# Optimization experiments

Measured on AMD Instinct MI355X. Metric: run time of the kernel, lower is better.

## Reference

```python
import jax, jax.numpy as jnp
import numpy as np

D_MODEL = 1024
N_HEADS = 16
SEQ = 2048
BATCH = 2
EPS = 1e-5


def layer_norm(x, g, b):
    mu = jnp.mean(x, axis=-1, keepdims=True)
    var = jnp.mean(jnp.square(x - mu), axis=-1, keepdims=True)
    return (x - mu) * jax.lax.rsqrt(var + EPS) * g + b


def setup_inputs() -> dict:
    key = jax.random.key(0)
    ks = jax.random.split(key, 10)
    D = D_MODEL
    s = lambda fan_in: 1.0 / np.sqrt(fan_in)
    return {
        "x": jax.random.normal(ks[0], (BATCH, SEQ, D), dtype=jnp.float32),
        # weights stored [in, out] (torch Linear is y = x @ W.T; equivalent math)
        "w_attn": jax.random.uniform(ks[1], (D, 3 * D), minval=-s(D), maxval=s(D), dtype=jnp.float32),
        "b_attn": jnp.zeros((3 * D,), jnp.float32),
        "w_proj": jax.random.uniform(ks[2], (D, D), minval=-s(D), maxval=s(D), dtype=jnp.float32),
        "b_proj": jnp.zeros((D,), jnp.float32),
        "ln1_g": jnp.ones((D,), jnp.float32),
        "ln1_b": jnp.zeros((D,), jnp.float32),
        "ln2_g": jnp.ones((D,), jnp.float32),
        "ln2_b": jnp.zeros((D,), jnp.float32),
        "w_fc1": jax.random.uniform(ks[3], (D, 4 * D), minval=-s(D), maxval=s(D), dtype=jnp.float32),
        "b_fc1": jnp.zeros((4 * D,), jnp.float32),
        "w_fc2": jax.random.uniform(ks[4], (4 * D, D), minval=-s(4 * D), maxval=s(4 * D), dtype=jnp.float32),
        "b_fc2": jnp.zeros((D,), jnp.float32),
    }


def reference(x, w_attn, b_attn, w_proj, b_proj, ln1_g, ln1_b, ln2_g, ln2_b, w_fc1, b_fc1, w_fc2, b_fc2):
    B, L, D = x.shape
    H = N_HEADS
    Dh = D // H

    # --- attention sublayer ---
    h = layer_norm(x, ln1_g, ln1_b)
    qkv = h @ w_attn + b_attn                      # [B, L, 3D]
    # SOURCE BUG (faithful): q, k, v are all taken from the k third.
    k = qkv[..., D:2 * D]
    kh = k.reshape(B, L, H, Dh).transpose(0, 2, 1, 3)   # [B, H, L, Dh]
    att = jnp.einsum('bhqd,bhkd->bhqk', kh, kh) / jnp.sqrt(jnp.float32(Dh))
    att = jax.nn.softmax(att, axis=-1)
    out = jnp.einsum('bhqk,bhkd->bhqd', att, kh)         # [B, H, L, Dh]
    out = out.transpose(0, 2, 1, 3).reshape(B, L, D)
    x = x + (out @ w_proj + b_proj)

    # --- feed-forward sublayer ---
    h = layer_norm(x, ln2_g, ln2_b)
    h = jax.nn.relu(h @ w_fc1 + b_fc1)
    x = x + (h @ w_fc2 + b_fc2)
    return x
```

## Files before the change

### kernel.cpp

```cpp
#include <hip/hip_runtime.h>


typedef __attribute__((ext_vector_type(8))) short s8v;
typedef __attribute__((ext_vector_type(4))) short s4v;
typedef __attribute__((ext_vector_type(4))) float f4v;

#define D_MODEL 1024
#define SEQ 2048
#define BATCH 2
#define NH 16
#define DH 64
#define MROWS (BATCH * SEQ)

#define KH_SCALE 0.42466088f
#define KH_ISCALE 2.3548200f

__device__ __forceinline__ float b2f(unsigned short u) {
  union { unsigned int i; float f; } v; v.i = ((unsigned int)u) << 16; return v.f;
}
__device__ __forceinline__ unsigned short f2b(float f) {
  unsigned int i = __builtin_bit_cast(unsigned int, f);
  unsigned int r = (i + 0x7fffu + ((i >> 16) & 1u)) >> 16;
  return (unsigned short)r;
}
__device__ __forceinline__ void async16(const void* g, void* l) {
  __builtin_amdgcn_global_load_lds(
      (const __attribute__((address_space(1))) unsigned int*)g,
      (__attribute__((address_space(3))) unsigned int*)l, 16, 0, 0);
}
__device__ __forceinline__ unsigned short cvt_b(float f) { return f2b(f); }
__device__ __forceinline__ unsigned short cvt_b(unsigned short u) { return u; }

__device__ __forceinline__ float xp2(float x) {
#if __has_builtin(__builtin_amdgcn_exp2f)
  return __builtin_amdgcn_exp2f(x);
#else
  return exp2f(x);
#endif
}

__device__ __forceinline__ s4v cvt4(float a, float b, float c, float d) {
  unsigned int lo, hi;
  asm("v_cvt_pk_bf16_f32 %0, %1, %2" : "=v"(lo) : "v"(a), "v"(b));
  asm("v_cvt_pk_bf16_f32 %0, %1, %2" : "=v"(hi) : "v"(c), "v"(d));
  union { unsigned long long u; s4v v; } u;
  u.u = ((unsigned long long)hi << 32) | (unsigned long long)lo;
  return u.v;
}

#if __has_builtin(__builtin_amdgcn_mfma_f32_16x16x16_bf16)
__device__ __forceinline__ f4v mfma16(s4v a, s4v b, f4v c) {
  return __builtin_amdgcn_mfma_f32_16x16x16_bf16(a, b, c, 0, 0, 0);
}
#elif __has_builtin(__builtin_amdgcn_mfma_f32_16x16x16bf16_1k)
__device__ __forceinline__ f4v mfma16(s4v a, s4v b, f4v c) {
  return __builtin_amdgcn_mfma_f32_16x16x16bf16_1k(a, b, c, 0, 0, 0);
}
#else
__device__ __forceinline__ f4v mfma16(s4v a, s4v b, f4v c) {
  s8v aa = {a[0], a[1], a[2], a[3], 0, 0, 0, 0};
  s8v bb = {b[0], b[1], b[2], b[3], 0, 0, 0, 0};
  return __builtin_amdgcn_mfma_f32_16x16x32_bf16(aa, bb, c, 0, 0, 0);
}
#endif

__global__ __launch_bounds__(256) void ln_kernel(
    const float* __restrict__ x, const float* __restrict__ g,
    const float* __restrict__ bb, unsigned short* __restrict__ out) {
  int row = blockIdx.x;
  int t = threadIdx.x;
  const float* xr = x + (size_t)row * D_MODEL;
  float v[4];
  float s = 0.f, s2 = 0.f;
#pragma unroll
  for (int i = 0; i < 4; ++i) {
    float f = xr[t + 256 * i];
    v[i] = f; s += f; s2 += f * f;
  }
#pragma unroll
  for (int off = 1; off < 64; off <<= 1) {
    s += __shfl_xor(s, off, 64);
    s2 += __shfl_xor(s2, off, 64);
  }
  __shared__ float red[8];
  if ((t & 63) == 0) { red[t >> 6] = s; red[4 + (t >> 6)] = s2; }
  __syncthreads();
  s = red[0] + red[1] + red[2] + red[3];
  s2 = red[4] + red[5] + red[6] + red[7];
  float mu = s * (1.f / D_MODEL);
  float var = s2 * (1.f / D_MODEL) - mu * mu;
  float rstd = rsqrtf(var + 1e-5f);
#pragma unroll
  for (int i = 0; i < 4; ++i) {
    int c = t + 256 * i;
    float h = (v[i] - mu) * rstd * g[c] + bb[c];
    out[(size_t)row * D_MODEL + c] = f2b(h);
  }
}

template <typename T>
__global__ __launch_bounds__(256) void transpose_b(
    const T* __restrict__ src, unsigned short* __restrict__ dst,
    int srcStride, int dstStride, long long srcBatch, long long dstBatch) {
  __shared__ unsigned short tile[64][65];
  const T* s = src + (size_t)blockIdx.z * srcBatch;
  unsigned short* d = dst + (size_t)blockIdx.z * dstBatch;
  int n0 = blockIdx.x * 64, k0 = blockIdx.y * 64;
  for (int i = threadIdx.x; i < 4096; i += 256) {
    int k = i >> 6, n = i & 63;
    tile[k][n] = cvt_b(s[(size_t)(k0 + k) * srcStride + n0 + n]);
  }
  __syncthreads();
  for (int i = threadIdx.x; i < 4096; i += 256) {
    int n = i >> 6, k = i & 63;
    d[(size_t)(n0 + n) * dstStride + k0 + k] = tile[k][n];
  }
}

template <int RES, bool RELU, bool KH, int OUTF, int BM, int BN>
__global__ __launch_bounds__(256) void gemm_bt(
    const unsigned short* __restrict__ A, const unsigned short* __restrict__ Bt,
    const float* __restrict__ bias, const float* __restrict__ res,
    void* __restrict__ out, int M, int N, int K) {
  constexpr int MT = BM / 32;
  constexpr int NT = BN / 32;
  __shared__ __align__(16) unsigned short lsA[2][BM * 64];
  __shared__ __align__(16) unsigned short lsB[2][BN * 64];
  int tid = threadIdx.x;
  int lane = tid & 63, w = tid >> 6, quad = lane >> 4, l16 = lane & 15;
  int m0 = blockIdx.y * BM, n0 = blockIdx.x * BN;
  int wm = (w >> 1) * (BM / 2), wn = (w & 1) * (BN / 2);
  f4v acc[MT][NT] = {};

  auto stage = [&](int bsel, int ktE) {
#pragma unroll
    for (int i = 0; i < MT; ++i) {
      int cb = w * (BM * 2) + i * 64;
      int ci = cb + lane;
      int row = ci >> 3, c = ci & 7;
      int cs = c ^ (row & 7);
      async16(A + (size_t)(m0 + row) * K + ktE + cs * 8, &lsA[bsel][cb * 8]);
    }
#pragma unroll
    for (int i = 0; i < NT; ++i) {
      int cb = w * (BN * 2) + i * 64;
      int ci = cb + lane;
      int row = ci >> 3, c = ci & 7;
      int cs = c ^ (row & 7);
      async16(Bt + (size_t)(n0 + row) * K + ktE + cs * 8, &lsB[bsel][cb * 8]);
    }
  };

  stage(0, 0);
  int nK = K >> 6;
  for (int kt = 0; kt < nK; ++kt) {
    int b = kt & 1;
    if (kt + 1 < nK) {
      stage(b ^ 1, (kt + 1) << 6);
      if constexpr (MT + NT == 4)      asm volatile("s_waitcnt vmcnt(4)" ::: "memory");
      else if constexpr (MT + NT == 6) asm volatile("s_waitcnt vmcnt(6)" ::: "memory");
      else                             asm volatile("s_waitcnt vmcnt(8)" ::: "memory");
    } else {
      asm volatile("s_waitcnt vmcnt(0)" ::: "memory");
    }
    __builtin_amdgcn_sched_barrier(0);
    __builtin_amdgcn_s_barrier();
    __builtin_amdgcn_sched_barrier(0);
#pragma unroll
    for (int s = 0; s < 2; ++s) {
      s8v af[MT], bf[NT];
#pragma unroll
      for (int t = 0; t < MT; ++t) {
        int am = wm + t * 16 + l16;
        int ac = (s * 4 + quad) ^ (am & 7);
        af[t] = *(const s8v*)(&lsA[b][am * 64 + ac * 8]);
      }
#pragma unroll
      for (int t = 0; t < NT; ++t) {
        int bn = wn + t * 16 + l16;
        int bc = (s * 4 + quad) ^ (bn & 7);
        bf[t] = *(const s8v*)(&lsB[b][bn * 64 + bc * 8]);
      }
#pragma unroll
      for (int ti = 0; ti < MT; ++ti)
#pragma unroll
        for (int tj = 0; tj < NT; ++tj)
          acc[ti][tj] = __builtin_amdgcn_mfma_f32_16x16x32_bf16(
              af[ti], bf[tj], acc[ti][tj], 0, 0, 0);
    }
    asm volatile("s_waitcnt lgkmcnt(0)" ::: "memory");
    __builtin_amdgcn_sched_barrier(0);
    __builtin_amdgcn_s_barrier();
    __builtin_amdgcn_sched_barrier(0);
  }
#pragma unroll
  for (int tj = 0; tj < NT; ++tj) {
    int col = n0 + wn + tj * 16 + l16;
    float bv = bias[col];
#pragma unroll
    for (int ti = 0; ti < MT; ++ti) {
#pragma unroll
      for (int r = 0; r < 4; ++r) {
        int rowg = m0 + wm + ti * 16 + quad * 4 + r;
        float vv = acc[ti][tj][r] + bv;
        if (KH) vv *= KH_SCALE;
        if (RES == 2) vv += res[(size_t)rowg * N + col];
        if (RELU) vv = fmaxf(vv, 0.f);
        size_t oidx;
        if (KH) {
          int b2 = rowg >> 11, l = rowg & 2047, h = col >> 6, d = col & 63;
          oidx = (((size_t)(b2 * NH + h)) * SEQ + l) * DH + d;
        } else {
          oidx = (size_t)rowg * N + col;
        }
        if (OUTF == 0) ((unsigned short*)out)[oidx] = f2b(vv);
        else           ((float*)out)[oidx] = vv;
      }
    }
  }
}

__global__ __launch_bounds__(256) void flash_k(
    const unsigned short* __restrict__ kh, const unsigned short* __restrict__ khT,
    unsigned short* __restrict__ Opart, float* __restrict__ lpart) {
  __shared__ __align__(16) unsigned short lsK[128 * 64];
  __shared__ __align__(16) unsigned short lsKT[64 * 128];
  int tid = threadIdx.x;
  int lane = tid & 63, w = tid >> 6, quad = lane >> 4, l16 = lane & 15;
  int split = blockIdx.x, bh = blockIdx.y, qb = blockIdx.z;
  const unsigned short* khB = kh + (size_t)bh * SEQ * DH;
  const unsigned short* khTB = khT + (size_t)bh * DH * SEQ;
  unsigned short* Op = Opart + (size_t)split * MROWS * D_MODEL;
  float* lp = lpart + (size_t)split * BATCH * NH * SEQ;
  s8v aQ[2][2];
#pragma unroll
  for (int g = 0; g < 2; ++g) {
    int q = qb * 128 + w * 32 + g * 16 + l16;
#pragma unroll
    for (int s = 0; s < 2; ++s)
      aQ[g][s] = *(const s8v*)(khB + (size_t)q * DH + s * 32 + quad * 8);
  }
  const s4v vone = {(short)0x3F80, (short)0x3F80, (short)0x3F80, (short)0x3F80};
  f4v accO[2][4] = {};
  f4v accL[2] = {};

  for (int kt8 = 0; kt8 < 8; ++kt8) {
    int key0 = split * 1024 + kt8 * 128;
#pragma unroll
    for (int i = 0; i < 4; ++i) {
      int cb = w * 256 + i * 64;
      int ci = cb + lane;
      int row = ci >> 3, c = ci & 7;
      int cs = c ^ (row & 7);
      async16(khB + (size_t)(key0 + row) * DH + cs * 8, &lsK[cb * 8]);
    }
#pragma unroll
    for (int i = 0; i < 4; ++i) {
      int cb = w * 256 + i * 64;
      int ci = cb + lane;
      int row = ci >> 4, c = ci & 15;
      int cs = c ^ (row & 15);
      async16(khTB + (size_t)row * SEQ + key0 + cs * 8, &lsKT[cb * 8]);
    }
    __builtin_amdgcn_s_waitcnt(0x0f70);
    __syncthreads();
#pragma unroll
    for (int half = 0; half < 2; ++half) {
      f4v accST[2][4] = {};
#pragma unroll
      for (int s = 0; s < 2; ++s) {
#pragma unroll
        for (int tj = 0; tj < 4; ++tj) {
          int key = half * 64 + tj * 16 + l16;
          int c = (s * 4 + quad) ^ (key & 7);
          s8v kf = *(const s8v*)(&lsK[key * 64 + c * 8]);
#pragma unroll
          for (int g = 0; g < 2; ++g)
            accST[g][tj] = __builtin_amdgcn_mfma_f32_16x16x32_bf16(
                kf, aQ[g][s], accST[g][tj], 0, 0, 0);
        }
      }
#pragma unroll
      for (int tj = 0; tj < 4; ++tj) {
        s4v pf[2];
#pragma unroll
        for (int g = 0; g < 2; ++g) {
          float p0 = xp2(accST[g][tj][0]);
          float p1 = xp2(accST[g][tj][1]);
          float p2 = xp2(accST[g][tj][2]);
          float p3 = xp2(accST[g][tj][3]);
          pf[g] = cvt4(p0, p1, p2, p3);
          accL[g] = mfma16(pf[g], vone, accL[g]);
        }
#pragma unroll
        for (int db = 0; db < 4; ++db) {
          int d = db * 16 + l16;
          int ch = (half * 8 + tj * 2 + (quad >> 1)) ^ (d & 15);
          s4v vf = *(const s4v*)(&lsKT[d * 128 + ch * 8 + (quad & 1) * 4]);
#pragma unroll
          for (int g = 0; g < 2; ++g)
            accO[g][db] = mfma16(pf[g], vf, accO[g][db]);
        }
      }
    }
    __syncthreads();
  }
  int b = bh >> 4, h = bh & 15;
#pragma unroll
  for (int g = 0; g < 2; ++g) {
    if (l16 == 0) {
#pragma unroll
      for (int r = 0; r < 4; ++r) {
        int q = qb * 128 + w * 32 + g * 16 + quad * 4 + r;
        lp[(size_t)bh * SEQ + q] = accL[g][r];
      }
    }
#pragma unroll
    for (int r = 0; r < 4; ++r) {
      int l = qb * 128 + w * 32 + g * 16 + quad * 4 + r;
#pragma unroll
      for (int db = 0; db < 4; ++db) {
        int d = db * 16 + l16;
        Op[((size_t)(b * SEQ + l)) * D_MODEL + h * DH + d] = f2b(accO[g][db][r]);
      }
    }
  }
}

__global__ __launch_bounds__(256) void attn_combine(
    const unsigned short* __restrict__ Opart, const float* __restrict__ lpart,
    unsigned short* __restrict__ attn) {
  int row = blockIdx.x;
  int b = row >> 11, l = row & 2047;
  int c0 = threadIdx.x * 4;
  int h = c0 >> 6;
  size_t lidx = (size_t)(b * NH + h) * SEQ + l;
  float ls = lpart[lidx] + lpart[(size_t)BATCH * NH * SEQ + lidx];
  float inv = KH_ISCALE / ls;
  s4v o0 = *(const s4v*)(Opart + (size_t)row * D_MODEL + c0);
  s4v o1 = *(const s4v*)(Opart + (size_t)MROWS * D_MODEL +
                         (size_t)row * D_MODEL + c0);
  s4v ov;
#pragma unroll
  for (int i = 0; i < 4; ++i)
    ov[i] = (short)f2b((b2f((unsigned short)o0[i]) +
                        b2f((unsigned short)o1[i])) * inv);
  *(s4v*)(attn + (size_t)row * D_MODEL + c0) = ov;
}

extern "C" void kernel_launch(void* const* d_in, const int* in_sizes, int n_in,
                              void* d_out, int out_size, void* d_ws, size_t ws_size,
                              hipStream_t stream) {
  (void)in_sizes; (void)n_in; (void)out_size;
  const float* x      = (const float*)d_in[0];
  const float* w_attn = (const float*)d_in[1];
  const float* b_attn = (const float*)d_in[2];
  const float* w_proj = (const float*)d_in[3];
  const float* b_proj = (const float*)d_in[4];
  const float* ln1_g  = (const float*)d_in[5];
  const float* ln1_b  = (const float*)d_in[6];
  const float* ln2_g  = (const float*)d_in[7];
  const float* ln2_b  = (const float*)d_in[8];
  const float* w_fc1  = (const float*)d_in[9];
  const float* b_fc1  = (const float*)d_in[10];
  const float* w_fc2  = (const float*)d_in[11];
  const float* b_fc2  = (const float*)d_in[12];

  char* ws = (char*)d_ws;
  float*          x1    = (float*)(ws);
  unsigned short* hbuf  = (unsigned short*)(ws + (size_t)(16u << 20));
  unsigned short* wT1   = (unsigned short*)(ws + (size_t)(24u << 20));
  unsigned short* wT2   = (unsigned short*)(ws + (size_t)(32u << 20));
  unsigned short* kh    = (unsigned short*)(ws + (size_t)(40u << 20));
  unsigned short* khT   = (unsigned short*)(ws + (size_t)(48u << 20));
  unsigned short* Opart = (unsigned short*)(ws);
  float*          lpart = (float*)(ws + (size_t)(16u << 20));
  unsigned short* fc1o  = kh;
  unsigned short* attn  = (unsigned short*)d_out;
  float* outf = (float*)d_out;
  bool big_ws = ws_size >= ((size_t)72u << 20);

  dim3 blk(256);
  hipLaunchKernelGGL(ln_kernel, dim3(MROWS), blk, 0, stream, x, ln1_g, ln1_b, hbuf);
  hipLaunchKernelGGL(transpose_b<float>, dim3(16, 16, 1), blk, 0, stream,
                     w_attn + 1024, wT1, 3 * D_MODEL, D_MODEL, 0LL, 0LL);
  hipLaunchKernelGGL((gemm_bt<0, false, true, 0, 64, 64>), dim3(16, 64), blk, 0,
                     stream, hbuf, wT1, b_attn + 1024, nullptr, (void*)kh,
                     MROWS, D_MODEL, D_MODEL);
  hipLaunchKernelGGL(transpose_b<unsigned short>, dim3(1, 32, 32), blk, 0, stream,
                     kh, khT, DH, SEQ, (long long)(SEQ * DH), (long long)(DH * SEQ));
  hipLaunchKernelGGL(flash_k, dim3(2, 32, SEQ / 128), blk, 0, stream,
                     kh, khT, Opart, lpart);
  hipLaunchKernelGGL(attn_combine, dim3(MROWS), blk, 0, stream,
                     Opart, lpart, attn);
  hipLaunchKernelGGL(transpose_b<float>, dim3(16, 16, 1), blk, 0, stream,
                     w_proj, wT1, D_MODEL, D_MODEL, 0LL, 0LL);
  hipLaunchKernelGGL((gemm_bt<2, false, false, 1, 64, 64>), dim3(16, 64), blk, 0,
                     stream, attn, wT1, b_proj, x, (void*)x1,
                     MROWS, D_MODEL, D_MODEL);
  hipLaunchKernelGGL(ln_kernel, dim3(MROWS), blk, 0, stream, x1, ln2_g, ln2_b, hbuf);
  hipLaunchKernelGGL(transpose_b<float>, dim3(64, 16, 1), blk, 0, stream,
                     w_fc1, wT1, 4 * D_MODEL, D_MODEL, 0LL, 0LL);
  hipLaunchKernelGGL(transpose_b<float>, dim3(16, 64, 1), blk, 0, stream,
                     w_fc2, wT2, D_MODEL, 4 * D_MODEL, 0LL, 0LL);
  if (big_ws) {
    hipLaunchKernelGGL((gemm_bt<0, true, false, 0, 128, 64>), dim3(64, 32), blk, 0,
                       stream, hbuf, wT1, b_fc1, nullptr, (void*)fc1o,
                       MROWS, 4 * D_MODEL, D_MODEL);
    hipLaunchKernelGGL((gemm_bt<2, false, false, 1, 64, 64>), dim3(16, 64), blk, 0,
                       stream, fc1o, wT2, b_fc2, x1, (void*)outf,
                       MROWS, D_MODEL, 4 * D_MODEL);
  } else {
    for (int c = 0; c < 2; ++c) {
      const unsigned short* h2c = hbuf + (size_t)c * 2048 * D_MODEL;
      const float* x1c = x1 + (size_t)c * 2048 * D_MODEL;
      float* outc = outf + (size_t)c * 2048 * D_MODEL;
      hipLaunchKernelGGL((gemm_bt<0, true, false, 0, 128, 64>), dim3(64, 16), blk, 0,
                         stream, h2c, wT1, b_fc1, nullptr, (void*)fc1o,
                         2048, 4 * D_MODEL, D_MODEL);
      hipLaunchKernelGGL((gemm_bt<2, false, false, 1, 64, 64>), dim3(16, 32), blk, 0,
                         stream, fc1o, wT2, b_fc2, x1c, (void*)outc,
                         2048, D_MODEL, 4 * D_MODEL);
    }
  }
}
```

Before: 339.8 us.

## Fuse attention split combine into projection GEMM and add XCD block swizzle

Removes the separate attn_combine kernel. The new projection GEMM loads both flash-attention partial outputs and their row sums, normalises them in registers and writes bf16 tiles to LDS before the MFMA step, so the intermediate attention buffer no longer takes a global round trip. GEMM block indices are also remapped so consecutive tiles land on the same XCD for better L2 reuse, and the workspace layout is reorganised to fit. The cost is more global loads per K-step in the projection GEMM, issued synchronously rather than with async LDS copies, which may reduce its pipelining efficiency.

Result: no change. 341.5 us (+0.5%).

```diff
diff --git a/kernel.cpp b/kernel.cpp
--- a/kernel.cpp
+++ b/kernel.cpp
@@ -63,6 +63,10 @@
   return __builtin_amdgcn_mfma_f32_16x16x32_bf16(aa, bb, c, 0, 0, 0);
 }
 #endif
+
+__device__ __forceinline__ int xcd_swz(int bidl, int nwg) {
+  return (nwg & 7) ? bidl : ((bidl & 7) * (nwg >> 3) + (bidl >> 3));
+}
 
 __global__ __launch_bounds__(256) void ln_kernel(
     const float* __restrict__ x, const float* __restrict__ g,
@@ -128,7 +132,9 @@
   __shared__ __align__(16) unsigned short lsB[2][BN * 64];
   int tid = threadIdx.x;
   int lane = tid & 63, w = tid >> 6, quad = lane >> 4, l16 = lane & 15;
-  int m0 = blockIdx.y * BM, n0 = blockIdx.x * BN;
+  int bidl = blockIdx.y * (int)gridDim.x + blockIdx.x;
+  int swz = xcd_swz(bidl, (int)(gridDim.x * gridDim.y));
+  int m0 = (swz / (int)gridDim.x) * BM, n0 = (swz % (int)gridDim.x) * BN;
   int wm = (w >> 1) * (BM / 2), wn = (w & 1) * (BN / 2);
   f4v acc[MT][NT] = {};
 
@@ -220,6 +226,140 @@
   }
 }
 
+__global__ __launch_bounds__(256) void gemm_proj(
+    const unsigned short* __restrict__ Opart, const float* __restrict__ lpart,
+    const unsigned short* __restrict__ Bt, const float* __restrict__ bias,
+    const float* __restrict__ res, float* __restrict__ out, int M, int N, int K) {
+  __shared__ __align__(16) unsigned short lsA[2][64 * 64];
+  __shared__ __align__(16) unsigned short lsB[2][64 * 64];
+  int tid = threadIdx.x;
+  int lane = tid & 63, w = tid >> 6, quad = lane >> 4, l16 = lane & 15;
+  int bidl = blockIdx.y * (int)gridDim.x + blockIdx.x;
+  int swz = xcd_swz(bidl, (int)(gridDim.x * gridDim.y));
+  int m0 = (swz / (int)gridDim.x) * 64, n0 = (swz % (int)gridDim.x) * 64;
+  int wm = (w >> 1) * 32, wn = (w & 1) * 32;
+  f4v acc[2][2] = {};
+
+  int ci_[2], csA[2], mA[2], b2A[2], lA[2];
+#pragma unroll
+  for (int i = 0; i < 2; ++i) {
+    int cb = w * 128 + i * 64;
+    int ci = cb + lane;
+    int row = ci >> 3, c = ci & 7;
+    ci_[i] = ci; csA[i] = c ^ (row & 7);
+    mA[i] = m0 + row; b2A[i] = mA[i] >> 11; lA[i] = mA[i] & 2047;
+  }
+  s8v o0r[2], o1r[2];
+  float lsr0[2], lsr1[2];
+  auto issueA = [&](int kt) {
+#pragma unroll
+    for (int i = 0; i < 2; ++i) {
+      const unsigned short* pa =
+          Opart + (size_t)mA[i] * D_MODEL + kt * 64 + csA[i] * 8;
+      o0r[i] = *(const s8v*)pa;
+      o1r[i] = *(const s8v*)(pa + (size_t)MROWS * D_MODEL);
+      size_t lidx = ((size_t)b2A[i] * NH + kt) * SEQ + lA[i];
+      lsr0[i] = lpart[lidx];
+      lsr1[i] = lpart[(size_t)BATCH * NH * SEQ + lidx];
+    }
+  };
+  auto issueB = [&](int bsel, int ktE) {
+#pragma unroll
+    for (int i = 0; i < 2; ++i) {
+      int cb = w * 128 + i * 64;
+      int ci = cb + lane;
+      int row = ci >> 3, c = ci & 7;
+      int cs = c ^ (row & 7);
+      async16(Bt + (size_t)(n0 + row) * K + ktE + cs * 8, &lsB[bsel][cb * 8]);
+    }
+  };
+  auto combineWrite = [&](int bsel) {
+#pragma unroll
+    for (int i = 0; i < 2; ++i) {
+      float inv = KH_ISCALE / (lsr0[i] + lsr1[i]);
+      float f[8];
+#pragma unroll
+      for (int j = 0; j < 8; ++j)
+        f[j] = (b2f((unsigned short)o0r[i][j]) +
+                b2f((unsigned short)o1r[i][j])) * inv;
+      s4v lo = cvt4(f[0], f[1], f[2], f[3]);
+      s4v hi = cvt4(f[4], f[5], f[6], f[7]);
+      s8v vv = {lo[0], lo[1], lo[2], lo[3], hi[0], hi[1], hi[2], hi[3]};
+      *(s8v*)(&lsA[bsel][ci_[i] * 8]) = vv;
+    }
+  };
+
+  issueA(0); issueB(0, 0);
+  __builtin_amdgcn_sched_barrier(0);
+  asm volatile("s_waitcnt vmcnt(2)" ::: "memory");
+  __builtin_amdgcn_sched_barrier(0);
+  combineWrite(0);
+  asm volatile("s_waitcnt lgkmcnt(0)" ::: "memory");
+  __builtin_amdgcn_sched_barrier(0);
+
+  int nK = K >> 6;
+  for (int kt = 0; kt < nK; ++kt) {
+    int b = kt & 1;
+    if (kt + 1 < nK) {
+      issueA(kt + 1); issueB(b ^ 1, (kt + 1) << 6);
+      __builtin_amdgcn_sched_barrier(0);
+      asm volatile("s_waitcnt vmcnt(10)" ::: "memory");
+    } else {
+      __builtin_amdgcn_sched_barrier(0);
+      asm volatile("s_waitcnt vmcnt(0)" ::: "memory");
+    }
+    __builtin_amdgcn_sched_barrier(0);
+    __builtin_amdgcn_s_barrier();
+    __builtin_amdgcn_sched_barrier(0);
+#pragma unroll
+    for (int s = 0; s < 2; ++s) {
+      s8v af[2], bf[2];
+#pragma unroll
+      for (int t = 0; t < 2; ++t) {
+        int am = wm + t * 16 + l16;
+        int ac = (s * 4 + quad) ^ (am & 7);
+        af[t] = *(const s8v*)(&lsA[b][am * 64 + ac * 8]);
+      }
+#pragma unroll
+      for (int t = 0; t < 2; ++t) {
+        int bn = wn + t * 16 + l16;
+        int bc = (s * 4 + quad) ^ (bn & 7);
+        bf[t] = *(const s8v*)(&lsB[b][bn * 64 + bc * 8]);
+      }
+#pragma unroll
+      for (int ti = 0; ti < 2; ++ti)
+#pragma unroll
+        for (int tj = 0; tj < 2; ++tj)
+          acc[ti][tj] = __builtin_amdgcn_mfma_f32_16x16x32_bf16(
+              af[ti], bf[tj], acc[ti][tj], 0, 0, 0);
+    }
+    if (kt + 1 < nK) {
+      __builtin_amdgcn_sched_barrier(0);
+      asm volatile("s_waitcnt vmcnt(2)" ::: "memory");
+      __builtin_amdgcn_sched_barrier(0);
+      combineWrite(b ^ 1);
+    }
+    asm volatile("s_waitcnt lgkmcnt(0)" ::: "memory");
+    __builtin_amdgcn_sched_barrier(0);
+    __builtin_amdgcn_s_barrier();
+    __builtin_amdgcn_sched_barrier(0);
+  }
+#pragma unroll
+  for (int tj = 0; tj < 2; ++tj) {
+    int col = n0 + wn + tj * 16 + l16;
+    float bv = bias[col];
+#pragma unroll
+    for (int ti = 0; ti < 2; ++ti) {
+#pragma unroll
+      for (int r = 0; r < 4; ++r) {
+        int rowg = m0 + wm + ti * 16 + quad * 4 + r;
+        float vv = acc[ti][tj][r] + bv + res[(size_t)rowg * N + col];
+        out[(size_t)rowg * N + col] = vv;
+      }
+    }
+  }
+}
+
 __global__ __launch_bounds__(256) void flash_k(
     const unsigned short* __restrict__ kh, const unsigned short* __restrict__ khT,
     unsigned short* __restrict__ Opart, float* __restrict__ lpart) {
@@ -325,27 +465,6 @@
       }
     }
   }
-}
-
-__global__ __launch_bounds__(256) void attn_combine(
-    const unsigned short* __restrict__ Opart, const float* __restrict__ lpart,
-    unsigned short* __restrict__ attn) {
-  int row = blockIdx.x;
-  int b = row >> 11, l = row & 2047;
-  int c0 = threadIdx.x * 4;
-  int h = c0 >> 6;
-  size_t lidx = (size_t)(b * NH + h) * SEQ + l;
-  float ls = lpart[lidx] + lpart[(size_t)BATCH * NH * SEQ + lidx];
-  float inv = KH_ISCALE / ls;
-  s4v o0 = *(const s4v*)(Opart + (size_t)row * D_MODEL + c0);
-  s4v o1 = *(const s4v*)(Opart + (size_t)MROWS * D_MODEL +
-                         (size_t)row * D_MODEL + c0);
-  s4v ov;
-#pragma unroll
-  for (int i = 0; i < 4; ++i)
-    ov[i] = (short)f2b((b2f((unsigned short)o0[i]) +
-                        b2f((unsigned short)o1[i])) * inv);
-  *(s4v*)(attn + (size_t)row * D_MODEL + c0) = ov;
 }
 
 extern "C" void kernel_launch(void* const* d_in, const int* in_sizes, int n_in,
@@ -367,48 +486,61 @@
   const float* b_fc2  = (const float*)d_in[12];
 
   char* ws = (char*)d_ws;
-  float*          x1    = (float*)(ws);
-  unsigned short* hbuf  = (unsigned short*)(ws + (size_t)(16u << 20));
-  unsigned short* wT1   = (unsigned short*)(ws + (size_t)(24u << 20));
-  unsigned short* wT2   = (unsigned short*)(ws + (size_t)(32u << 20));
-  unsigned short* kh    = (unsigned short*)(ws + (size_t)(40u << 20));
-  unsigned short* khT   = (unsigned short*)(ws + (size_t)(48u << 20));
-  unsigned short* Opart = (unsigned short*)(ws);
-  float*          lpart = (float*)(ws + (size_t)(16u << 20));
-  unsigned short* fc1o  = kh;
-  unsigned short* attn  = (unsigned short*)d_out;
+  unsigned short* Opart = (unsigned short*)ws;
+  unsigned short* kh    = (unsigned short*)(ws + (size_t)(16u << 20));
+  unsigned short* khT   = (unsigned short*)(ws + (size_t)(24u << 20));
+  float*          x1    = (float*)(ws + (size_t)(32u << 20));
+  unsigned short* hbuf  = (unsigned short*)(ws + (size_t)(48u << 20));
+  float*          lpart = (float*)(ws + (size_t)(48u << 20));
   float* outf = (float*)d_out;
   bool big_ws = ws_size >= ((size_t)72u << 20);
+
+  unsigned short* wTk;
+  unsigned short* wTp;
+  unsigned short* wTf1;
+  unsigned short* wTf2;
+  unsigned short* fc1o;
+  if (big_ws) {
+    wTk  = (unsigned short*)(ws + (size_t)(56u << 20));
+    wTp  = wTk;
+    wTf1 = wTk;
+    wTf2 = (unsigned short*)(ws + (size_t)(64u << 20));
+    fc1o = (unsigned short*)ws;
+  } else {
+    wTk  = (unsigned short*)ws;
+    wTp  = kh;
+    wTf1 = (unsigned short*)ws;
+    wTf2 = (unsigned short*)(ws + (size_t)(8u << 20));
+    fc1o = kh;
+  }
 
   dim3 blk(256);
   hipLaunchKernelGGL(ln_kernel, dim3(MROWS), blk, 0, stream, x, ln1_g, ln1_b, hbuf);
   hipLaunchKernelGGL(transpose_b<float>, dim3(16, 16, 1), blk, 0, stream,
-                     w_attn + 1024, wT1, 3 * D_MODEL, D_MODEL, 0LL, 0LL);
+                     w_attn + 1024, wTk, 3 * D_MODEL, D_MODEL, 0LL, 0LL);
   hipLaunchKernelGGL((gemm_bt<0, false, true, 0, 64, 64>), dim3(16, 64), blk, 0,
-                     stream, hbuf, wT1, b_attn + 1024, nullptr, (void*)kh,
+                     stream, hbuf, wTk, b_attn + 1024, nullptr, (void*)kh,
                      MROWS, D_MODEL, D_MODEL);
   hipLaunchKernelGGL(transpose_b<unsigned short>, dim3(1, 32, 32), blk, 0, stream,
                      kh, khT, DH, SEQ, (long long)(SEQ * DH), (long long)(DH * SEQ));
   hipLaunchKernelGGL(flash_k, dim3(2, 32, SEQ / 128), blk, 0, stream,
                      kh, khT, Opart, lpart);
-  hipLaunchKernelGGL(attn_combine, dim3(MROWS), blk, 0, stream,
-                     Opart, lpart, attn);
   hipLaunchKernelGGL(transpose_b<float>, dim3(16, 16, 1), blk, 0, stream,
-                     w_proj, wT1, D_MODEL, D_MODEL, 0LL, 0LL);
-  hipLaunchKernelGGL((gemm_bt<2, false, false, 1, 64, 64>), dim3(16, 64), blk, 0,
-                     stream, attn, wT1, b_proj, x, (void*)x1,
+                     w_proj, wTp, D_MODEL, D_MODEL, 0LL, 0LL);
+  hipLaunchKernelGGL(gemm_proj, dim3(16, 64), blk, 0, stream,
+                     Opart, lpart, wTp, b_proj, x, x1,
                      MROWS, D_MODEL, D_MODEL);
   hipLaunchKernelGGL(ln_kernel, dim3(MROWS), blk, 0, stream, x1, ln2_g, ln2_b, hbuf);
   hipLaunchKernelGGL(transpose_b<float>, dim3(64, 16, 1), blk, 0, stream,
-                     w_fc1, wT1, 4 * D_MODEL, D_MODEL, 0LL, 0LL);
+                     w_fc1, wTf1, 4 * D_MODEL, D_MODEL, 0LL, 0LL);
   hipLaunchKernelGGL(transpose_b<float>, dim3(16, 64, 1), blk, 0, stream,
-                     w_fc2, wT2, D_MODEL, 4 * D_MODEL, 0LL, 0LL);
+                     w_fc2, wTf2, D_MODEL, 4 * D_MODEL, 0LL, 0LL);
   if (big_ws) {
     hipLaunchKernelGGL((gemm_bt<0, true, false, 0, 128, 64>), dim3(64, 32), blk, 0,
-                       stream, hbuf, wT1, b_fc1, nullptr, (void*)fc1o,
+                       stream, hbuf, wTf1, b_fc1, nullptr, (void*)fc1o,
                        MROWS, 4 * D_MODEL, D_MODEL);
     hipLaunchKernelGGL((gemm_bt<2, false, false, 1, 64, 64>), dim3(16, 64), blk, 0,
-                       stream, fc1o, wT2, b_fc2, x1, (void*)outf,
+                       stream, fc1o, wTf2, b_fc2, x1, (void*)outf,
                        MROWS, D_MODEL, 4 * D_MODEL);
   } else {
     for (int c = 0; c < 2; ++c) {
@@ -416,10 +548,10 @@
       const float* x1c = x1 + (size_t)c * 2048 * D_MODEL;
       float* outc = outf + (size_t)c * 2048 * D_MODEL;
       hipLaunchKernelGGL((gemm_bt<0, true, false, 0, 128, 64>), dim3(64, 16), blk, 0,
-                         stream, h2c, wT1, b_fc1, nullptr, (void*)fc1o,
+                         stream, h2c, wTf1, b_fc1, nullptr, (void*)fc1o,
                          2048, 4 * D_MODEL, D_MODEL);
       hipLaunchKernelGGL((gemm_bt<2, false, false, 1, 64, 64>), dim3(16, 32), blk, 0,
-                         stream, fc1o, wT2, b_fc2, x1c, (void*)outc,
+                         stream, fc1o, wTf2, b_fc2, x1c, (void*)outc,
                          2048, D_MODEL, 4 * D_MODEL);
     }
   }
```
